# Kernel optimization log

Hardware: AMD Instinct MI355X
Metric: run time of the kernel (lower is better)

Reference implementation:

```python
import jax, jax.numpy as jnp
import numpy as np

N_QUBITS = 5
N_A = 1
Q_DEPTH = 6
PATCH = 2 ** (N_QUBITS - N_A)  # 16


def _cz_sign(w):
    # diagonal sign of CZ on wires (w, w+1) over a (2,)*N_QUBITS state grid
    s = np.ones((2,) * N_QUBITS, np.float32)
    idx = [slice(None)] * N_QUBITS
    idx[w] = 1
    idx[w + 1] = 1
    s[tuple(idx)] = -1.0
    return jnp.asarray(s)

CZ_SIGNS = [_cz_sign(w) for w in range(N_QUBITS - 1)]


def apply_ry(state, theta, wire):
    # state: (B, 2,2,2,2,2) real amplitudes; theta: scalar or (B,)
    c = jnp.cos(theta * 0.5)
    s = jnp.sin(theta * 0.5)
    if jnp.ndim(c) == 1:  # per-sample angle
        c = c[:, None, None, None, None]
        s = s[:, None, None, None, None]
    st = jnp.moveaxis(state, 1 + wire, -1)
    a0, a1 = st[..., 0], st[..., 1]
    out = jnp.stack([c * a0 - s * a1, s * a0 + c * a1], axis=-1)
    return jnp.moveaxis(out, -1, 1 + wire)


def run_generator(noise, weights):
    # noise: (B, 5) per-sample angles; weights: (6, 5) shared angles
    B = noise.shape[0]
    state = jnp.zeros((B,) + (2,) * N_QUBITS, noise.dtype)
    state = state.at[(slice(None),) + (0,) * N_QUBITS].set(1.0)  # |00000>
    for w in range(N_QUBITS):
        state = apply_ry(state, noise[:, w], w)
    for d in range(Q_DEPTH):
        for w in range(N_QUBITS):
            state = apply_ry(state, weights[d, w], w)
        for w in range(N_QUBITS - 1):
            state = state * CZ_SIGNS[w]
    # RY/CZ are real, so probs = amplitude^2; unitary => sum(probs)=1
    probs = state.reshape(B, 2 ** N_QUBITS) ** 2
    p0 = probs[:, :PATCH]
    p0 = p0 / jnp.sum(probs, axis=1, keepdims=True)
    return p0 / jnp.max(p0, axis=1, keepdims=True)


def setup_inputs() -> dict:
    key = jax.random.key(0)
    k1, k2 = jax.random.split(key)
    B, C, H, W = 262144, 1, 4, 4
    inp = jax.random.normal(k1, (B, C, H, W), dtype=jnp.float32)
    q_params = jax.random.uniform(k2, (4, Q_DEPTH * N_QUBITS), dtype=jnp.float32)  # q_delta=1
    return {"input": inp, "q_params": q_params}


def reference(input, q_params):
    B, C, H, W = input.shape
    k = 2  # scale_factor
    # bilinear (half-pixel / align_corners=False) upsample
    up = jax.image.resize(input, (B, C, H * k, W * k), method='linear')
    noise = up.reshape(B, -1)[:, :N_QUBITS]  # 5 angles per sample
    outs = [run_generator(noise, q_params[g].reshape(Q_DEPTH, N_QUBITS))
            for g in range(q_params.shape[0])]
    return jnp.concatenate(outs, axis=1)  # (B, n_generators * 16)
```

## Files before the change

kernel.cpp:

```cpp
#include <hip/hip_runtime.h>

#define NQ   5
#define QD   6
#define NGEN 4
#define NW   (NGEN * QD * NQ)

typedef float f32x4 __attribute__((ext_vector_type(4)));
typedef short short8 __attribute__((ext_vector_type(8)));

__device__ inline unsigned short f2bf_rne(float f) {
    unsigned u = __float_as_uint(f);
    u += 0x7FFFu + ((u >> 16) & 1u);
    return (unsigned short)(u >> 16);
}
__device__ inline float bf2f(unsigned short h) {
    return __uint_as_float(((unsigned)h) << 16);
}

__global__ __launch_bounds__(128) void qsrgan_build(
    const float* __restrict__ qp,
    unsigned short* __restrict__ Mh,
    unsigned short* __restrict__ Ml)
{
    __shared__ float cw[NW];
    __shared__ float sw[NW];
    const int t = threadIdx.x;
    if (t < NW) {
        float sv, cv;
        __sincosf(0.5f * qp[t], &sv, &cv);
        cw[t] = cv;
        sw[t] = sv;
    }
    __syncthreads();

    const int g = t >> 5;
    const int basis = t & 31;

    float st[32];
#pragma unroll
    for (int i = 0; i < 32; ++i) st[i] = (i == basis) ? 1.0f : 0.0f;

    for (int d = 0; d < QD; ++d) {
        const int base = g * (QD * NQ) + d * NQ;
#pragma unroll
        for (int w = 0; w < NQ; ++w) {
            const float cc = cw[base + w];
            const float ss = sw[base + w];
            const int stride = 1 << (4 - w);
#pragma unroll
            for (int i = 0; i < 32; ++i) {
                if (i & stride) continue;
                float a0 = st[i];
                float a1 = st[i + stride];
                st[i]          = cc * a0 - ss * a1;
                st[i + stride] = ss * a0 + cc * a1;
            }
        }
#pragma unroll
        for (int i = 0; i < 32; ++i) {
            int flips = 0;
#pragma unroll
            for (int w = 0; w < NQ - 1; ++w) {
                const int m = (1 << (4 - w)) | (1 << (3 - w));
                flips ^= ((i & m) == m) ? 1 : 0;
            }
            if (flips) st[i] = -st[i];
        }
    }

#pragma unroll
    for (int j = 0; j < 16; ++j) {
        const float v = st[j];
        const unsigned short hi = f2bf_rne(v);
        const float r = v - bf2f(hi);
        const unsigned short lo = f2bf_rne(r);
        const int idx = ((g * 4 + (basis >> 3)) * 16 + j) * 8 + (basis & 7);
        Mh[idx] = hi;
        Ml[idx] = lo;
    }
}

__global__ __launch_bounds__(256, 4) void qsrgan_apply(
    const float* __restrict__ inp,
    const unsigned short* __restrict__ Mh,
    const unsigned short* __restrict__ Ml,
    float* __restrict__ out,
    int B)
{
    const int t    = threadIdx.x;
    const int lane = t & 63;
    const int w    = t >> 6;
    const int q    = lane >> 4;
    const int c    = lane & 15;
    const int s0   = blockIdx.x * 64;

    const int bsmp = min(s0 + w * 16 + c, B - 1);
    const float4 x = *reinterpret_cast<const float4*>(inp + (size_t)bsmp * 16);

    short8 mh[4], ml[4];
    const short8* gh = reinterpret_cast<const short8*>(Mh);
    const short8* gl = reinterpret_cast<const short8*>(Ml);
#pragma unroll
    for (int g = 0; g < 4; ++g) {
        mh[g] = gh[g * 64 + lane];
        ml[g] = gl[g * 64 + lane];
    }

    float n[5];
    n[0] = x.x;
    n[1] = 0.75f * x.x + 0.25f * x.y;
    n[2] = 0.25f * x.x + 0.75f * x.y;
    n[3] = 0.75f * x.y + 0.25f * x.z;
    n[4] = 0.25f * x.y + 0.75f * x.z;
    float cn[5], sn[5];
#pragma unroll
    for (int i = 0; i < 5; ++i) __sincosf(0.5f * n[i], &sn[i], &cn[i]);

    const float U = ((q >> 1) ? sn[0] : cn[0]) * ((q & 1) ? sn[1] : cn[1]);
    float w34[4];
    w34[0] = cn[3] * cn[4];
    w34[1] = cn[3] * sn[4];
    w34[2] = sn[3] * cn[4];
    w34[3] = sn[3] * sn[4];

    short8 ih, il;
#pragma unroll
    for (int j = 0; j < 8; ++j) {
        const float a = U * ((j >> 2) ? sn[2] : cn[2]) * w34[j & 3];
        const unsigned short hi = f2bf_rne(a);
        const float r = a - bf2f(hi);
        ih[j] = (short)hi;
        il[j] = (short)f2bf_rne(r);
    }

    f32x4 acc[4];
#pragma unroll
    for (int g = 0; g < 4; ++g) {
        f32x4 a0 = {0.0f, 0.0f, 0.0f, 0.0f};
        a0 = __builtin_amdgcn_mfma_f32_16x16x32_bf16(mh[g], ih, a0, 0, 0, 0);
        a0 = __builtin_amdgcn_mfma_f32_16x16x32_bf16(ml[g], ih, a0, 0, 0, 0);
        a0 = __builtin_amdgcn_mfma_f32_16x16x32_bf16(mh[g], il, a0, 0, 0, 0);
        acc[g] = a0;
    }

    float* __restrict__ orow = out + (size_t)bsmp * 64;
#pragma unroll
    for (int g = 0; g < 4; ++g) {
        float p0 = acc[g][0] * acc[g][0];
        float p1 = acc[g][1] * acc[g][1];
        float p2 = acc[g][2] * acc[g][2];
        float p3 = acc[g][3] * acc[g][3];
        float m = fmaxf(fmaxf(p0, p1), fmaxf(p2, p3));
        m = fmaxf(m, __shfl_xor(m, 16));
        m = fmaxf(m, __shfl_xor(m, 32));
        const float inv = 1.0f / m;
        float4 v = make_float4(p0 * inv, p1 * inv, p2 * inv, p3 * inv);
        *reinterpret_cast<float4*>(orow + g * 16 + q * 4) = v;
    }
}

extern "C" void kernel_launch(void* const* d_in, const int* in_sizes, int n_in,
                              void* d_out, int out_size, void* d_ws, size_t ws_size,
                              hipStream_t stream) {
    const float* inp = (const float*)d_in[0];
    const float* qp  = (const float*)d_in[1];
    float* out = (float*)d_out;
    unsigned short* Mh = (unsigned short*)d_ws;
    unsigned short* Ml = (unsigned short*)d_ws + 2048;
    const int B = in_sizes[0] / 16;

    qsrgan_build<<<1, 128, 0, stream>>>(qp, Mh, Ml);
    const int blocks = (B + 63) / 64;
    qsrgan_apply<<<blocks, 256, 0, stream>>>(inp, Mh, Ml, out, B);
}
```

Baseline: 91.83 us.

## Switch generator matmul to 32x32x16 MFMA with 32 samples per wave

Replaces the 16x16x32 bf16 MFMA path with 32x32x16 MFMAs, so each wave handles 32 samples instead of 16 and each block covers 128 samples. The unitary matrices are re-laid out in the build kernel to fit the new operand format, and the input amplitudes are split into two K-halves. This halves the grid size and the per-sample instruction overhead (input loads, sincos, matrix loads), at the cost of more accumulator registers and a different output store pattern with strided float4 writes.

Result: no change. 90.26 us (-1.7%).

```diff
diff --git a/kernel.cpp b/kernel.cpp
--- a/kernel.cpp
+++ b/kernel.cpp
@@ -5,8 +5,8 @@
 #define NGEN 4
 #define NW   (NGEN * QD * NQ)
 
-typedef float f32x4 __attribute__((ext_vector_type(4)));
-typedef short short8 __attribute__((ext_vector_type(8)));
+typedef float  f32x16 __attribute__((ext_vector_type(16)));
+typedef short  short8 __attribute__((ext_vector_type(8)));
 
 __device__ inline unsigned short f2bf_rne(float f) {
     unsigned u = __float_as_uint(f);
@@ -68,13 +68,18 @@
         }
     }
 
-#pragma unroll
-    for (int j = 0; j < 16; ++j) {
-        const float v = st[j];
+    const int T = g >> 1;
+    const int S = basis >> 4;
+    const int lane_h = 32 * ((basis >> 3) & 1);
+    const int j = basis & 7;
+#pragma unroll
+    for (int ch = 0; ch < 16; ++ch) {
+        const float v = st[ch];
         const unsigned short hi = f2bf_rne(v);
         const float r = v - bf2f(hi);
         const unsigned short lo = f2bf_rne(r);
-        const int idx = ((g * 4 + (basis >> 3)) * 16 + j) * 8 + (basis & 7);
+        const int m   = (g & 1) * 16 + ch;
+        const int idx = (((T * 2 + S) * 64) + (m + lane_h)) * 8 + j;
         Mh[idx] = hi;
         Ml[idx] = lo;
     }
@@ -90,20 +95,20 @@
     const int t    = threadIdx.x;
     const int lane = t & 63;
     const int w    = t >> 6;
-    const int q    = lane >> 4;
-    const int c    = lane & 15;
-    const int s0   = blockIdx.x * 64;
-
-    const int bsmp = min(s0 + w * 16 + c, B - 1);
+    const int s    = lane & 31;
+    const int h    = lane >> 5;
+    const int s0   = blockIdx.x * 128 + w * 32;
+
+    const int bsmp = min(s0 + s, B - 1);
     const float4 x = *reinterpret_cast<const float4*>(inp + (size_t)bsmp * 16);
 
     short8 mh[4], ml[4];
     const short8* gh = reinterpret_cast<const short8*>(Mh);
     const short8* gl = reinterpret_cast<const short8*>(Ml);
 #pragma unroll
-    for (int g = 0; g < 4; ++g) {
-        mh[g] = gh[g * 64 + lane];
-        ml[g] = gl[g * 64 + lane];
+    for (int i = 0; i < 4; ++i) {
+        mh[i] = gh[i * 64 + lane];
+        ml[i] = gl[i * 64 + lane];
     }
 
     float n[5];
@@ -116,46 +121,73 @@
 #pragma unroll
     for (int i = 0; i < 5; ++i) __sincosf(0.5f * n[i], &sn[i], &cn[i]);
 
-    const float U = ((q >> 1) ? sn[0] : cn[0]) * ((q & 1) ? sn[1] : cn[1]);
     float w34[4];
     w34[0] = cn[3] * cn[4];
     w34[1] = cn[3] * sn[4];
     w34[2] = sn[3] * cn[4];
     w34[3] = sn[3] * sn[4];
-
-    short8 ih, il;
-#pragma unroll
-    for (int j = 0; j < 8; ++j) {
-        const float a = U * ((j >> 2) ? sn[2] : cn[2]) * w34[j & 3];
-        const unsigned short hi = f2bf_rne(a);
-        const float r = a - bf2f(hi);
-        ih[j] = (short)hi;
-        il[j] = (short)f2bf_rne(r);
-    }
-
-    f32x4 acc[4];
-#pragma unroll
-    for (int g = 0; g < 4; ++g) {
-        f32x4 a0 = {0.0f, 0.0f, 0.0f, 0.0f};
-        a0 = __builtin_amdgcn_mfma_f32_16x16x32_bf16(mh[g], ih, a0, 0, 0, 0);
-        a0 = __builtin_amdgcn_mfma_f32_16x16x32_bf16(ml[g], ih, a0, 0, 0, 0);
-        a0 = __builtin_amdgcn_mfma_f32_16x16x32_bf16(mh[g], il, a0, 0, 0, 0);
-        acc[g] = a0;
+    float w234[8];
+#pragma unroll
+    for (int j = 0; j < 8; ++j)
+        w234[j] = ((j >> 2) ? sn[2] : cn[2]) * w34[j & 3];
+
+    const float w1 = h ? sn[1] : cn[1];
+    const float pre[2] = { cn[0] * w1, sn[0] * w1 };
+
+    short8 ih[2], il[2];
+#pragma unroll
+    for (int S = 0; S < 2; ++S) {
+#pragma unroll
+        for (int j = 0; j < 8; ++j) {
+            const float a = pre[S] * w234[j];
+            const unsigned short hi = f2bf_rne(a);
+            const float r = a - bf2f(hi);
+            ih[S][j] = (short)hi;
+            il[S][j] = (short)f2bf_rne(r);
+        }
+    }
+
+    f32x16 acc[2];
+#pragma unroll
+    for (int T = 0; T < 2; ++T) {
+        f32x16 a;
+#pragma unroll
+        for (int r = 0; r < 16; ++r) a[r] = 0.0f;
+#pragma unroll
+        for (int S = 0; S < 2; ++S) {
+            const int i = T * 2 + S;
+            a = __builtin_amdgcn_mfma_f32_32x32x16_bf16(mh[i], ih[S], a, 0, 0, 0);
+            a = __builtin_amdgcn_mfma_f32_32x32x16_bf16(ml[i], ih[S], a, 0, 0, 0);
+            a = __builtin_amdgcn_mfma_f32_32x32x16_bf16(mh[i], il[S], a, 0, 0, 0);
+        }
+        acc[T] = a;
     }
 
     float* __restrict__ orow = out + (size_t)bsmp * 64;
 #pragma unroll
-    for (int g = 0; g < 4; ++g) {
-        float p0 = acc[g][0] * acc[g][0];
-        float p1 = acc[g][1] * acc[g][1];
-        float p2 = acc[g][2] * acc[g][2];
-        float p3 = acc[g][3] * acc[g][3];
-        float m = fmaxf(fmaxf(p0, p1), fmaxf(p2, p3));
-        m = fmaxf(m, __shfl_xor(m, 16));
-        m = fmaxf(m, __shfl_xor(m, 32));
-        const float inv = 1.0f / m;
-        float4 v = make_float4(p0 * inv, p1 * inv, p2 * inv, p3 * inv);
-        *reinterpret_cast<float4*>(orow + g * 16 + q * 4) = v;
+    for (int T = 0; T < 2; ++T) {
+        float p[16];
+#pragma unroll
+        for (int r = 0; r < 16; ++r) p[r] = acc[T][r] * acc[T][r];
+
+        float mlo = fmaxf(fmaxf(fmaxf(p[0], p[1]), fmaxf(p[2], p[3])),
+                          fmaxf(fmaxf(p[4], p[5]), fmaxf(p[6], p[7])));
+        float mhi = fmaxf(fmaxf(fmaxf(p[8], p[9]), fmaxf(p[10], p[11])),
+                          fmaxf(fmaxf(p[12], p[13]), fmaxf(p[14], p[15])));
+        mlo = fmaxf(mlo, __shfl_xor(mlo, 32));
+        mhi = fmaxf(mhi, __shfl_xor(mhi, 32));
+        const float vlo = 1.0f / mlo;
+        const float vhi = 1.0f / mhi;
+
+        float4 v0 = make_float4(p[0] * vlo, p[1] * vlo, p[2] * vlo, p[3] * vlo);
+        float4 v1 = make_float4(p[4] * vlo, p[5] * vlo, p[6] * vlo, p[7] * vlo);
+        float4 v2 = make_float4(p[8] * vhi, p[9] * vhi, p[10] * vhi, p[11] * vhi);
+        float4 v3 = make_float4(p[12] * vhi, p[13] * vhi, p[14] * vhi, p[15] * vhi);
+        float* base = orow + T * 32 + 4 * h;
+        *reinterpret_cast<float4*>(base +  0) = v0;
+        *reinterpret_cast<float4*>(base +  8) = v1;
+        *reinterpret_cast<float4*>(base + 16) = v2;
+        *reinterpret_cast<float4*>(base + 24) = v3;
     }
 }
 
@@ -170,6 +202,6 @@
     const int B = in_sizes[0] / 16;
 
     qsrgan_build<<<1, 128, 0, stream>>>(qp, Mh, Ml);
-    const int blocks = (B + 63) / 64;
+    const int blocks = (B + 127) / 128;
     qsrgan_apply<<<blocks, 256, 0, stream>>>(inp, Mh, Ml, out, B);
 }
```
